# Performance work log

Hardware: AMD Instinct MI355X
Metric: run time of the kernel (lower is better)

Reference implementation:

```python
import jax, jax.numpy as jnp
import numpy as np

CAP_FACTOR = 1.25


def _moe_top1(x, wg, w1, b1, w2, b2):
    """Top-1 switch MoE with capacity-based token dropping.
    x: [T, d]; wg: [d, E]; w1: [E, d, f]; b1: [E, f]; w2: [E, f, d]; b2: [E, d].
    """
    T, d = x.shape
    E = wg.shape[1]
    cap = int(CAP_FACTOR * T / E)
    probs = jax.nn.softmax(x @ wg, axis=-1)            # [T, E]
    idx = jnp.argmax(probs, axis=-1)                   # [T] expert assignment
    gate = jnp.max(probs, axis=-1)                     # [T] gate prob
    oh = jax.nn.one_hot(idx, E, dtype=jnp.int32)       # [T, E]
    # position of each token within its expert's buffer
    pos = (jnp.cumsum(oh, axis=0) * oh).sum(-1) - 1    # [T]
    keep = pos < cap                                   # drop tokens over capacity
    pos_w = jnp.where(keep, pos, cap)                  # dropped -> overflow slot
    # dispatch: scatter tokens into per-expert buffers [E, cap+1, d]
    buf = jnp.zeros((E, cap + 1, d), dtype=x.dtype).at[idx, pos_w].set(x)
    buf = buf[:, :cap]                                 # slice off overflow slot
    # grouped expert FFN
    h = jax.nn.relu(jnp.einsum('ecd,edf->ecf', buf, w1) + b1[:, None, :])
    eo = jnp.einsum('ecf,efd->ecd', h, w2) + b2[:, None, :]
    # combine: gather each token's expert output, scale by gate prob, zero dropped
    pos_g = jnp.minimum(pos_w, cap - 1)
    out = eo[idx, pos_g] * (gate * keep.astype(x.dtype))[:, None]
    return out


def setup_inputs():
    key = jax.random.key(0)
    ks = jax.random.split(key, 12)
    B, S, d, dff, E1, E2 = 8, 2048, 1024, 4096, 8, 16
    s = lambda fan: np.float32(1.0 / np.sqrt(fan))
    return dict(
        x=jax.random.normal(ks[0], (B, S, d), jnp.float32),
        y=jax.random.randint(ks[1], (B,), 0, d),
        wg1=jax.random.normal(ks[2], (d, E1), jnp.float32) * s(d),
        w1a=jax.random.normal(ks[3], (E1, d, dff), jnp.float32) * s(d),
        b1a=jnp.zeros((E1, dff), jnp.float32),
        w2a=jax.random.normal(ks[4], (E1, dff, d), jnp.float32) * s(dff),
        b2a=jnp.zeros((E1, d), jnp.float32),
        wg2=jax.random.normal(ks[5], (d, E2), jnp.float32) * s(d),
        w1b=jax.random.normal(ks[6], (E2, d, dff), jnp.float32) * s(d),
        b1b=jnp.zeros((E2, dff), jnp.float32),
        w2b=jax.random.normal(ks[7], (E2, dff, d), jnp.float32) * s(dff),
        b2b=jnp.zeros((E2, d), jnp.float32),
    )


def reference(x, y, wg1, w1a, b1a, w2a, b2a, wg2, w1b, b1b, w2b, b2b):
    B, S, d = x.shape
    xf = x.reshape(B * S, d)
    m1 = _moe_top1(xf, wg1, w1a, b1a, w2a, b2a)        # moe1(x)
    m2 = _moe_top1(m1, wg2, w1b, b1b, w2b, b2b)        # moe2(moe_out)
    resid = x + m2.reshape(B, S, d)                    # residual add
    sent = resid.mean(axis=1)                          # [B, d] mean-pool -> logits
    logp = jax.nn.log_softmax(sent, axis=-1)
    return -logp[jnp.arange(B), y].mean()              # cross-entropy loss
```

## Files before the change

kernel.cpp:

```cpp
#include <hip/hip_runtime.h>
#include <hip/hip_bf16.h>
#include <cstdint>
#include <cstddef>

#define B_    8
#define S_    2048
#define D_    1024
#define DFF_  4096
#define E1_   8
#define E2_   16
#define T_    (B_*S_)
#define CAP1_ 2560
#define CAP2_ 1280
#define EC_   20480

typedef __bf16 bf16x8 __attribute__((ext_vector_type(8)));
typedef float  f32x4  __attribute__((ext_vector_type(4)));

__device__ __forceinline__ unsigned short f2bf(float x) {
  return __builtin_bit_cast(unsigned short, (__bf16)x);
}

#define SB0 __builtin_amdgcn_sched_barrier(0)
#define VM0 asm volatile("s_waitcnt vmcnt(0)" ::: "memory")

template<int E>
__global__ __launch_bounds__(256)
void gate_kernel(const float* __restrict__ X, const float* __restrict__ WG,
                 int* __restrict__ idxO, float* __restrict__ gateO) {
  const int lane = threadIdx.x & 63;
  const int wv   = threadIdx.x >> 6;
  const int t    = blockIdx.x * 4 + wv;
  const float* xr = X + (size_t)t * D_;
  float acc[E];
#pragma unroll
  for (int e = 0; e < E; ++e) acc[e] = 0.f;
#pragma unroll
  for (int i = 0; i < 4; ++i) {
    float4 xv = *(const float4*)(xr + i * 256 + lane * 4);
    int kb = i * 256 + lane * 4;
#pragma unroll
    for (int j = 0; j < 4; ++j) {
      float xs = (&xv.x)[j];
      const float* wr = WG + (size_t)(kb + j) * E;
#pragma unroll
      for (int e = 0; e < E; ++e) acc[e] += xs * wr[e];
    }
  }
#pragma unroll
  for (int e = 0; e < E; ++e) {
    float v = acc[e];
#pragma unroll
    for (int s = 32; s >= 1; s >>= 1) v += __shfl_xor(v, s, 64);
    acc[e] = v;
  }
  if (lane == 0) {
    float mx = acc[0]; int mi = 0;
#pragma unroll
    for (int e = 1; e < E; ++e) if (acc[e] > mx) { mx = acc[e]; mi = e; }
    float s = 0.f;
#pragma unroll
    for (int e = 0; e < E; ++e) s += expf(acc[e] - mx);
    idxO[t]  = mi;
    gateO[t] = 1.0f / s;
  }
}

__global__ __launch_bounds__(1024)
void scan_kernel(const int* __restrict__ idx, int E, int cap,
                 int* __restrict__ pos, int* __restrict__ kept) {
  __shared__ int cnt[16][17];
  __shared__ int gbase[16];
  const int tid = threadIdx.x;
  const int w = tid >> 6, lane = tid & 63;
  if (tid < E) gbase[tid] = 0;
  __syncthreads();
  const unsigned long long lt = (lane == 63) ? 0xFFFFFFFFFFFFFFFFull >> 1
                                             : ((1ull << lane) - 1ull);
  for (int it = 0; it < T_ / 1024; ++it) {
    int t = it * 1024 + tid;
    int mi = idx[t];
    int rank = 0;
    for (int e = 0; e < E; ++e) {
      unsigned long long m = __ballot(mi == e);
      if (lane == 0) cnt[w][e] = __popcll(m);
      if (mi == e) rank = __popcll(m & lt);
    }
    __syncthreads();
    int off = 0;
    for (int w2 = 0; w2 < w; ++w2) off += cnt[w2][mi];
    pos[t] = gbase[mi] + off + rank;
    __syncthreads();
    if (tid < E) {
      int tot = 0;
      for (int w2 = 0; w2 < 16; ++w2) tot += cnt[w2][tid];
      gbase[tid] += tot;
    }
    __syncthreads();
  }
  if (tid < E) kept[tid] = min(gbase[tid], cap);
}

__global__ __launch_bounds__(64)
void scatter_kernel(const float* __restrict__ X, const int* __restrict__ idx,
                    const int* __restrict__ pos, int cap,
                    unsigned short* __restrict__ xbuf, int* __restrict__ tokmap,
                    float* __restrict__ mzero) {
  const int t = blockIdx.x;
  const int lane = threadIdx.x;
  const int p = pos[t];
  if (p < cap) {
    const size_t dst = ((size_t)idx[t] * cap + p) * D_;
    const float* xr = X + (size_t)t * D_;
#pragma unroll
    for (int i = 0; i < 4; ++i) {
      float4 v = *(const float4*)(xr + i * 256 + lane * 4);
      ushort4 o;
      o.x = f2bf(v.x); o.y = f2bf(v.y); o.z = f2bf(v.z); o.w = f2bf(v.w);
      *(ushort4*)(xbuf + dst + i * 256 + lane * 4) = o;
    }
    if (lane == 0) tokmap[(size_t)idx[t] * cap + p] = t;
  } else {
    float4 z = {0.f, 0.f, 0.f, 0.f};
    float* mr = mzero + (size_t)t * D_;
#pragma unroll
    for (int i = 0; i < 4; ++i) *(float4*)(mr + i * 256 + lane * 4) = z;
  }
}

__global__ __launch_bounds__(256)
void wtrans_kernel(const float* __restrict__ src, unsigned short* __restrict__ dst,
                   int K, int N) {
  __shared__ float t[64][65];
  const int tid = threadIdx.x;
  const size_t eo = (size_t)blockIdx.z * K * N;
  const int k0 = blockIdx.y * 64, n0 = blockIdx.x * 64;
  const float* s = src + eo + (size_t)k0 * N + n0;
  unsigned short* d = dst + eo + (size_t)n0 * K + k0;
#pragma unroll
  for (int i = 0; i < 4; ++i) {
    int k = i * 16 + (tid >> 4);
    int n4 = (tid & 15) * 4;
    float4 v = *(const float4*)(s + (size_t)k * N + n4);
    t[k][n4] = v.x; t[k][n4 + 1] = v.y; t[k][n4 + 2] = v.z; t[k][n4 + 3] = v.w;
  }
  __syncthreads();
#pragma unroll
  for (int i = 0; i < 4; ++i) {
    int n = i * 16 + (tid >> 4);
    int k4 = (tid & 15) * 4;
    ushort4 o;
    o.x = f2bf(t[k4][n]);     o.y = f2bf(t[k4 + 1][n]);
    o.z = f2bf(t[k4 + 2][n]); o.w = f2bf(t[k4 + 3][n]);
    *(ushort4*)(d + (size_t)n * K + k4) = o;
  }
}

template<int MODE>
__global__ __launch_bounds__(256, 2)
void moe_gemm(const unsigned short* __restrict__ A,
              const unsigned short* __restrict__ BT,
              const float* __restrict__ bias, int K, int N, int cap, int nbcnt,
              const int* __restrict__ kept,
              unsigned short* __restrict__ Hout, float* __restrict__ Mout,
              const int* __restrict__ tokmap, const float* __restrict__ gate,
              const float* __restrict__ tsrc, unsigned short* __restrict__ tdst,
              int tK, int tN, int tE, int tpb) {
  __shared__ char smem[65536];
  const int tid  = threadIdx.x;

  if (tsrc != nullptr) {
    float (*tt)[65] = (float(*)[65])smem;
    const int ntn = tN >> 6, ntk = tK >> 6;
    const int tiles = tE * ntk * ntn;
    int t0 = blockIdx.x * tpb;
    int t1 = t0 + tpb; if (t1 > tiles) t1 = tiles;
    for (int t = t0; t < t1; ++t) {
      const int e2 = t / (ntk * ntn), rem = t - e2 * (ntk * ntn);
      const int k0 = (rem / ntn) << 6, n0 = (rem - (rem / ntn) * ntn) << 6;
      const float* s = tsrc + (size_t)e2 * tK * tN + (size_t)k0 * tN + n0;
      unsigned short* d2 = tdst + (size_t)e2 * tK * tN + (size_t)n0 * tK + k0;
#pragma unroll
      for (int i = 0; i < 4; ++i) {
        int k = i * 16 + (tid >> 4);
        int n4 = (tid & 15) * 4;
        float4 v = *(const float4*)(s + (size_t)k * tN + n4);
        tt[k][n4] = v.x; tt[k][n4 + 1] = v.y; tt[k][n4 + 2] = v.z; tt[k][n4 + 3] = v.w;
      }
      __syncthreads();
#pragma unroll
      for (int i = 0; i < 4; ++i) {
        int n = i * 16 + (tid >> 4);
        int k4 = (tid & 15) * 4;
        ushort4 o;
        o.x = f2bf(tt[k4][n]);     o.y = f2bf(tt[k4 + 1][n]);
        o.z = f2bf(tt[k4 + 2][n]); o.w = f2bf(tt[k4 + 3][n]);
        *(ushort4*)(d2 + (size_t)n * tK + k4) = o;
      }
      __syncthreads();
    }
  }

  const int lane = tid & 63;
  const int wv   = tid >> 6;
  const int wr   = wv >> 1, wc = wv & 1;

  const int nwg = gridDim.x;
  const int wg  = (blockIdx.x & 7) * (nwg >> 3) + (blockIdx.x >> 3);
  const int per_grp = nbcnt * 8;
  const int grp = wg / per_grp;
  const int rem = wg - grp * per_grp;
  const int mb  = grp * 8 + (rem & 7);
  const int nb  = rem >> 3;

  const int e  = (mb * 128) / cap;
  const int r0 = mb * 128 - e * cap;
  const int kept_e = kept[e];
  if (r0 >= kept_e) return;
  const unsigned short* Ab = A + (size_t)(mb * 128) * K;
  const unsigned short* Bb = BT + ((size_t)e * N + (size_t)nb * 128) * K;

  f32x4 acc[4][4];
#pragma unroll
  for (int m = 0; m < 4; ++m)
#pragma unroll
    for (int n = 0; n < 4; ++n) acc[m][n] = (f32x4){0.f, 0.f, 0.f, 0.f};

  auto stage = [&](int buf, int k0) {
#pragma unroll
    for (int j = 0; j < 4; ++j) {
      const int c   = j * 256 + tid;
      const int row = c >> 3;
      const int cc  = c & 7;
      const int scol = (cc ^ (row & 7)) << 3;
      const unsigned short* ga = Ab + (size_t)row * K + k0 + scol;
      const unsigned short* gb = Bb + (size_t)row * K + k0 + scol;
      char* la = smem + buf * 32768 + (j * 256 + (tid & ~63)) * 16;
      char* lb = la + 16384;
      __builtin_amdgcn_global_load_lds((const __attribute__((address_space(1))) void*)ga,
                                       (__attribute__((address_space(3))) void*)la,
                                       16, 0, 0);
      __builtin_amdgcn_global_load_lds((const __attribute__((address_space(1))) void*)gb,
                                       (__attribute__((address_space(3))) void*)lb,
                                       16, 0, 0);
    }
  };

  const int NT = K >> 6;
  __syncthreads();
  stage(0, 0);
  __syncthreads();
  int cur = 0;

  const int g16 = (lane >> 4) * 16;
  const int r16 = lane & 15;

  for (int t = 0; t < NT; ++t) {
    if (t + 1 < NT) stage(cur ^ 1, (t + 1) << 6);

    const char* As = smem + cur * 32768;
    const char* Bs = As + 16384;
    bf16x8 af[4][2], bfr[4][2];
#pragma unroll
    for (int m = 0; m < 4; ++m) {
      const int row = wr * 64 + m * 16 + r16;
      const int sw  = (row & 7) << 4;
#pragma unroll
      for (int ks = 0; ks < 2; ++ks)
        af[m][ks] = *(const bf16x8*)(As + row * 128 + ((ks * 64 + g16) ^ sw));
    }
#pragma unroll
    for (int n = 0; n < 4; ++n) {
      const int row = wc * 64 + n * 16 + r16;
      const int sw  = (row & 7) << 4;
#pragma unroll
      for (int ks = 0; ks < 2; ++ks)
        bfr[n][ks] = *(const bf16x8*)(Bs + row * 128 + ((ks * 64 + g16) ^ sw));
    }
    __builtin_amdgcn_s_setprio(1);
#pragma unroll
    for (int ks = 0; ks < 2; ++ks)
#pragma unroll
      for (int m = 0; m < 4; ++m)
#pragma unroll
        for (int n = 0; n < 4; ++n)
          acc[m][n] = __builtin_amdgcn_mfma_f32_16x16x32_bf16(af[m][ks], bfr[n][ks], acc[m][n], 0, 0, 0);
    __builtin_amdgcn_s_setprio(0);
    __syncthreads();
    cur ^= 1;
  }

  const int rg = lane >> 4;
  float bv[4];
#pragma unroll
  for (int n = 0; n < 4; ++n)
    bv[n] = bias[(size_t)e * N + nb * 128 + wc * 64 + n * 16 + r16];

#pragma unroll
  for (int m = 0; m < 4; ++m) {
#pragma unroll
    for (int r = 0; r < 4; ++r) {
      const int lrow = wr * 64 + m * 16 + rg * 4 + r;
      if (MODE == 0) {
        unsigned short* orow = Hout + (size_t)(mb * 128 + lrow) * N + nb * 128;
#pragma unroll
        for (int n = 0; n < 4; ++n) {
          float v = acc[m][n][r] + bv[n];
          orow[wc * 64 + n * 16 + r16] = f2bf(fmaxf(v, 0.f));
        }
      } else {
        const int lr = r0 + lrow;
        if (lr < kept_e) {
          const int tok = tokmap[mb * 128 + lrow];
          const float gsc = gate[tok];
          float* orow = Mout + (size_t)tok * N + nb * 128;
#pragma unroll
          for (int n = 0; n < 4; ++n)
            orow[wc * 64 + n * 16 + r16] = (acc[m][n][r] + bv[n]) * gsc;
        }
      }
    }
  }
}

__global__ __launch_bounds__(256)
void reduce_kernel(const float* __restrict__ X, const float* __restrict__ M2,
                   float* __restrict__ sent) {
  const int c = blockIdx.x * 256 + threadIdx.x;
  const int b = blockIdx.z;
  const int s0 = blockIdx.y * 128;
  float a = 0.f;
  size_t base = ((size_t)b * S_ + s0) * D_ + c;
  for (int s = 0; s < 128; ++s) a += X[base + (size_t)s * D_] + M2[base + (size_t)s * D_];
  atomicAdd(&sent[b * D_ + c], a * (1.0f / (float)S_));
}

__global__ __launch_bounds__(64)
void loss_kernel(const float* __restrict__ sent, const int* __restrict__ y,
                 float* __restrict__ out) {
  const int lane = threadIdx.x;
  float total = 0.f;
  for (int b = 0; b < B_; ++b) {
    const float* s = sent + b * D_;
    float v[16];
    float mx = -1e30f;
#pragma unroll
    for (int i = 0; i < 16; ++i) { v[i] = s[lane + i * 64]; mx = fmaxf(mx, v[i]); }
#pragma unroll
    for (int sh = 32; sh >= 1; sh >>= 1) mx = fmaxf(mx, __shfl_xor(mx, sh, 64));
    float sm = 0.f;
#pragma unroll
    for (int i = 0; i < 16; ++i) sm += expf(v[i] - mx);
#pragma unroll
    for (int sh = 32; sh >= 1; sh >>= 1) sm += __shfl_xor(sm, sh, 64);
    total += logf(sm) + mx - s[y[b]];
  }
  if (lane == 0) out[0] = total * (1.0f / (float)B_);
}

extern "C" void kernel_launch(void* const* d_in, const int* in_sizes, int n_in,
                              void* d_out, int out_size, void* d_ws, size_t ws_size,
                              hipStream_t stream) {
  const float* x   = (const float*)d_in[0];
  const int*   y   = (const int*)d_in[1];
  const float* wg1 = (const float*)d_in[2];
  const float* w1a = (const float*)d_in[3];
  const float* b1a = (const float*)d_in[4];
  const float* w2a = (const float*)d_in[5];
  const float* b2a = (const float*)d_in[6];
  const float* wg2 = (const float*)d_in[7];
  const float* w1b = (const float*)d_in[8];
  const float* b1b = (const float*)d_in[9];
  const float* w2b = (const float*)d_in[10];
  const float* b2b = (const float*)d_in[11];
  float* out = (float*)d_out;
  (void)in_sizes; (void)n_in; (void)out_size;

  char* base = (char*)d_ws;
  size_t o = 0;
  auto alloc = [&](size_t bytes) { size_t r = o; o = (o + bytes + 255) & ~(size_t)255; return r; };
  int*   idx1    = (int*)  (base + alloc((size_t)T_ * 4));
  int*   pos1    = (int*)  (base + alloc((size_t)T_ * 4));
  float* gate1   = (float*)(base + alloc((size_t)T_ * 4));
  int*   idx2    = (int*)  (base + alloc((size_t)T_ * 4));
  int*   pos2    = (int*)  (base + alloc((size_t)T_ * 4));
  float* gate2   = (float*)(base + alloc((size_t)T_ * 4));
  int*   kept1   = (int*)  (base + alloc(64 * 4));
  int*   kept2   = (int*)  (base + alloc(64 * 4));
  int*   tokmap1 = (int*)  (base + alloc((size_t)EC_ * 4));
  int*   tokmap2 = (int*)  (base + alloc((size_t)EC_ * 4));
  float* sent    = (float*)(base + alloc((size_t)B_ * D_ * 4));
  float* m1      = (float*)(base + alloc((size_t)T_ * D_ * 4));
  unsigned short* xbuf = (unsigned short*)(base + alloc((size_t)EC_ * D_ * 2));
  unsigned short* h    = (unsigned short*)(base + alloc((size_t)EC_ * DFF_ * 2));
  unsigned short* P1   = (unsigned short*)(base + alloc((size_t)E2_ * D_ * DFF_ * 2));
  size_t need_with_P2 = o + (size_t)E2_ * D_ * DFF_ * 2 + 256;
  const bool fold = (ws_size >= need_with_P2);
  unsigned short* P2 = fold ? (unsigned short*)(base + alloc((size_t)E2_ * D_ * DFF_ * 2))
                            : P1;

  hipMemsetAsync(sent, 0, (size_t)B_ * D_ * 4, stream);

  const int G0 = (DFF_ / 128) * (EC_ / 128);
  const int G1 = (D_  / 128) * (EC_ / 128);
  const int TPB0 = (8192  + G0 - 1) / G0;
  const int TPB1 = (16384 + G1 - 1) / G1;
  const int TPB2 = (16384 + G0 - 1) / G0;

  gate_kernel<E1_><<<T_ / 4, 256, 0, stream>>>(x, wg1, idx1, gate1);
  scan_kernel<<<1, 1024, 0, stream>>>(idx1, E1_, CAP1_, pos1, kept1);
  scatter_kernel<<<T_, 64, 0, stream>>>(x, idx1, pos1, CAP1_, xbuf, tokmap1, m1);
  wtrans_kernel<<<dim3(DFF_ / 64, D_ / 64, E1_), 256, 0, stream>>>(w1a, P1, D_, DFF_);
  if (fold) {
    moe_gemm<0><<<G0, 256, 0, stream>>>(xbuf, P1, b1a, D_, DFF_, CAP1_, DFF_ / 128,
        kept1, h, nullptr, nullptr, nullptr, w2a, P2, DFF_, D_, E1_, TPB0);
    moe_gemm<1><<<G1, 256, 0, stream>>>(h, P2, b2a, DFF_, D_, CAP1_, D_ / 128,
        kept1, nullptr, m1, tokmap1, gate1, w1b, P1, D_, DFF_, E2_, TPB1);
  } else {
    moe_gemm<0><<<G0, 256, 0, stream>>>(xbuf, P1, b1a, D_, DFF_, CAP1_, DFF_ / 128,
        kept1, h, nullptr, nullptr, nullptr, nullptr, nullptr, 0, 0, 0, 0);
    wtrans_kernel<<<dim3(D_ / 64, DFF_ / 64, E1_), 256, 0, stream>>>(w2a, P2, DFF_, D_);
    moe_gemm<1><<<G1, 256, 0, stream>>>(h, P2, b2a, DFF_, D_, CAP1_, D_ / 128,
        kept1, nullptr, m1, tokmap1, gate1, nullptr, nullptr, 0, 0, 0, 0);
    wtrans_kernel<<<dim3(DFF_ / 64, D_ / 64, E2_), 256, 0, stream>>>(w1b, P1, D_, DFF_);
  }

  gate_kernel<E2_><<<T_ / 4, 256, 0, stream>>>(m1, wg2, idx2, gate2);
  scan_kernel<<<1, 1024, 0, stream>>>(idx2, E2_, CAP2_, pos2, kept2);
  scatter_kernel<<<T_, 64, 0, stream>>>(m1, idx2, pos2, CAP2_, xbuf, tokmap2, m1);
  if (fold) {
    moe_gemm<0><<<G0, 256, 0, stream>>>(xbuf, P1, b1b, D_, DFF_, CAP2_, DFF_ / 128,
        kept2, h, nullptr, nullptr, nullptr, w2b, P2, DFF_, D_, E2_, TPB2);
    moe_gemm<1><<<G1, 256, 0, stream>>>(h, P2, b2b, DFF_, D_, CAP2_, D_ / 128,
        kept2, nullptr, m1, tokmap2, gate2, nullptr, nullptr, 0, 0, 0, 0);
  } else {
    moe_gemm<0><<<G0, 256, 0, stream>>>(xbuf, P1, b1b, D_, DFF_, CAP2_, DFF_ / 128,
        kept2, h, nullptr, nullptr, nullptr, nullptr, nullptr, 0, 0, 0, 0);
    wtrans_kernel<<<dim3(D_ / 64, DFF_ / 64, E2_), 256, 0, stream>>>(w2b, P2, DFF_, D_);
    moe_gemm<1><<<G1, 256, 0, stream>>>(h, P2, b2b, DFF_, D_, CAP2_, D_ / 128,
        kept2, nullptr, m1, tokmap2, gate2, nullptr, nullptr, 0, 0, 0, 0);
  }

  reduce_kernel<<<dim3(D_ / 256, S_ / 128, B_), 256, 0, stream>>>(x, m1, sent);
  loss_kernel<<<1, 64, 0, stream>>>(sent, y, out);
}
```

Before: 1.348 ms.

## Single-buffer GEMM LDS, raise occupancy, split weight transpose into dedicated blocks

The GEMM's LDS staging drops from double-buffered 64KB to single-buffered 32KB, and launch bounds go from 2 to 4 blocks per CU, trading load/compute overlap for more resident waves. The fused weight transpose now runs on 256 extra dedicated blocks placed at the front of the grid, each striding over tiles and then exiting. Previously every GEMM block did a small slice of the transpose before its matmul. The GEMM block index is rebased so tile mapping stays unchanged. Losing the prefetch double buffer may expose global load latency if the extra occupancy does not hide it.

```diff
diff --git a/kernel.cpp b/kernel.cpp
--- a/kernel.cpp
+++ b/kernel.cpp
@@ -20,9 +20,6 @@
 __device__ __forceinline__ unsigned short f2bf(float x) {
   return __builtin_bit_cast(unsigned short, (__bf16)x);
 }
-
-#define SB0 __builtin_amdgcn_sched_barrier(0)
-#define VM0 asm volatile("s_waitcnt vmcnt(0)" ::: "memory")
 
 template<int E>
 __global__ __launch_bounds__(256)
@@ -157,7 +154,7 @@
 }
 
 template<int MODE>
-__global__ __launch_bounds__(256, 2)
+__global__ __launch_bounds__(256, 4)
 void moe_gemm(const unsigned short* __restrict__ A,
               const unsigned short* __restrict__ BT,
               const float* __restrict__ bias, int K, int N, int cap, int nbcnt,
@@ -165,17 +162,15 @@
               unsigned short* __restrict__ Hout, float* __restrict__ Mout,
               const int* __restrict__ tokmap, const float* __restrict__ gate,
               const float* __restrict__ tsrc, unsigned short* __restrict__ tdst,
-              int tK, int tN, int tE, int tpb) {
-  __shared__ char smem[65536];
-  const int tid  = threadIdx.x;
-
-  if (tsrc != nullptr) {
+              int tK, int tN, int tE, int ntb) {
+  __shared__ char smem[32768];
+  const int tid = threadIdx.x;
+
+  if (tsrc != nullptr && (int)blockIdx.x < ntb) {
     float (*tt)[65] = (float(*)[65])smem;
     const int ntn = tN >> 6, ntk = tK >> 6;
     const int tiles = tE * ntk * ntn;
-    int t0 = blockIdx.x * tpb;
-    int t1 = t0 + tpb; if (t1 > tiles) t1 = tiles;
-    for (int t = t0; t < t1; ++t) {
+    for (int t = blockIdx.x; t < tiles; t += ntb) {
       const int e2 = t / (ntk * ntn), rem = t - e2 * (ntk * ntn);
       const int k0 = (rem / ntn) << 6, n0 = (rem - (rem / ntn) * ntn) << 6;
       const float* s = tsrc + (size_t)e2 * tK * tN + (size_t)k0 * tN + n0;
@@ -199,14 +194,16 @@
       }
       __syncthreads();
     }
-  }
-
+    return;
+  }
+
+  const int gbid = tsrc ? ((int)blockIdx.x - ntb) : (int)blockIdx.x;
+  const int ngb  = tsrc ? ((int)gridDim.x - ntb) : (int)gridDim.x;
   const int lane = tid & 63;
   const int wv   = tid >> 6;
   const int wr   = wv >> 1, wc = wv & 1;
 
-  const int nwg = gridDim.x;
-  const int wg  = (blockIdx.x & 7) * (nwg >> 3) + (blockIdx.x >> 3);
+  const int wg  = (gbid & 7) * (ngb >> 3) + (gbid >> 3);
   const int per_grp = nbcnt * 8;
   const int grp = wg / per_grp;
   const int rem = wg - grp * per_grp;
@@ -226,7 +223,7 @@
 #pragma unroll
     for (int n = 0; n < 4; ++n) acc[m][n] = (f32x4){0.f, 0.f, 0.f, 0.f};
 
-  auto stage = [&](int buf, int k0) {
+  auto stage = [&](int k0) {
 #pragma unroll
     for (int j = 0; j < 4; ++j) {
       const int c   = j * 256 + tid;
@@ -235,7 +232,7 @@
       const int scol = (cc ^ (row & 7)) << 3;
       const unsigned short* ga = Ab + (size_t)row * K + k0 + scol;
       const unsigned short* gb = Bb + (size_t)row * K + k0 + scol;
-      char* la = smem + buf * 32768 + (j * 256 + (tid & ~63)) * 16;
+      char* la = smem + (j * 256 + (tid & ~63)) * 16;
       char* lb = la + 16384;
       __builtin_amdgcn_global_load_lds((const __attribute__((address_space(1))) void*)ga,
                                        (__attribute__((address_space(3))) void*)la,
@@ -247,19 +244,15 @@
   };
 
   const int NT = K >> 6;
-  __syncthreads();
-  stage(0, 0);
-  __syncthreads();
-  int cur = 0;
-
   const int g16 = (lane >> 4) * 16;
   const int r16 = lane & 15;
 
   for (int t = 0; t < NT; ++t) {
-    if (t + 1 < NT) stage(cur ^ 1, (t + 1) << 6);
-
-    const char* As = smem + cur * 32768;
-    const char* Bs = As + 16384;
+    stage(t << 6);
+    __syncthreads();
+
+    const char* As = smem;
+    const char* Bs = smem + 16384;
     bf16x8 af[4][2], bfr[4][2];
 #pragma unroll
     for (int m = 0; m < 4; ++m) {
@@ -287,7 +280,6 @@
           acc[m][n] = __builtin_amdgcn_mfma_f32_16x16x32_bf16(af[m][ks], bfr[n][ks], acc[m][n], 0, 0, 0);
     __builtin_amdgcn_s_setprio(0);
     __syncthreads();
-    cur ^= 1;
   }
 
   const int rg = lane >> 4;
@@ -401,21 +393,19 @@
 
   hipMemsetAsync(sent, 0, (size_t)B_ * D_ * 4, stream);
 
-  const int G0 = (DFF_ / 128) * (EC_ / 128);
-  const int G1 = (D_  / 128) * (EC_ / 128);
-  const int TPB0 = (8192  + G0 - 1) / G0;
-  const int TPB1 = (16384 + G1 - 1) / G1;
-  const int TPB2 = (16384 + G0 - 1) / G0;
+  const int G0  = (DFF_ / 128) * (EC_ / 128);
+  const int G1  = (D_  / 128) * (EC_ / 128);
+  const int NTB = 256;
 
   gate_kernel<E1_><<<T_ / 4, 256, 0, stream>>>(x, wg1, idx1, gate1);
   scan_kernel<<<1, 1024, 0, stream>>>(idx1, E1_, CAP1_, pos1, kept1);
   scatter_kernel<<<T_, 64, 0, stream>>>(x, idx1, pos1, CAP1_, xbuf, tokmap1, m1);
   wtrans_kernel<<<dim3(DFF_ / 64, D_ / 64, E1_), 256, 0, stream>>>(w1a, P1, D_, DFF_);
   if (fold) {
-    moe_gemm<0><<<G0, 256, 0, stream>>>(xbuf, P1, b1a, D_, DFF_, CAP1_, DFF_ / 128,
-        kept1, h, nullptr, nullptr, nullptr, w2a, P2, DFF_, D_, E1_, TPB0);
-    moe_gemm<1><<<G1, 256, 0, stream>>>(h, P2, b2a, DFF_, D_, CAP1_, D_ / 128,
-        kept1, nullptr, m1, tokmap1, gate1, w1b, P1, D_, DFF_, E2_, TPB1);
+    moe_gemm<0><<<G0 + NTB, 256, 0, stream>>>(xbuf, P1, b1a, D_, DFF_, CAP1_, DFF_ / 128,
+        kept1, h, nullptr, nullptr, nullptr, w2a, P2, DFF_, D_, E1_, NTB);
+    moe_gemm<1><<<G1 + NTB, 256, 0, stream>>>(h, P2, b2a, DFF_, D_, CAP1_, D_ / 128,
+        kept1, nullptr, m1, tokmap1, gate1, w1b, P1, D_, DFF_, E2_, NTB);
   } else {
     moe_gemm<0><<<G0, 256, 0, stream>>>(xbuf, P1, b1a, D_, DFF_, CAP1_, DFF_ / 128,
         kept1, h, nullptr, nullptr, nullptr, nullptr, nullptr, 0, 0, 0, 0);
@@ -429,8 +419,8 @@
   scan_kernel<<<1, 1024, 0, stream>>>(idx2, E2_, CAP2_, pos2, kept2);
   scatter_kernel<<<T_, 64, 0, stream>>>(m1, idx2, pos2, CAP2_, xbuf, tokmap2, m1);
   if (fold) {
-    moe_gemm<0><<<G0, 256, 0, stream>>>(xbuf, P1, b1b, D_, DFF_, CAP2_, DFF_ / 128,
-        kept2, h, nullptr, nullptr, nullptr, w2b, P2, DFF_, D_, E2_, TPB2);
+    moe_gemm<0><<<G0 + NTB, 256, 0, stream>>>(xbuf, P1, b1b, D_, DFF_, CAP2_, DFF_ / 128,
+        kept2, h, nullptr, nullptr, nullptr, w2b, P2, DFF_, D_, E2_, NTB);
     moe_gemm<1><<<G1, 256, 0, stream>>>(h, P2, b2b, DFF_, D_, CAP2_, D_ / 128,
         kept2, nullptr, m1, tokmap2, gate2, nullptr, nullptr, 0, 0, 0, 0);
   } else {
```

New measurement: 2.753 ms. 2.04x slower.
